# Kernel tuning notes

Measured on AMD Instinct MI355X. Metric: run time of the kernel, lower is better.

The kernel has to match this reference:

```python
import jax, jax.numpy as jnp
import numpy as np

B, T, C = 4, 2048, 1024
H = 16
HD = C // H  # 64


def setup_inputs() -> dict:
    key = jax.random.key(0)
    k1, k2, k3, k4, k5 = jax.random.split(key, 5)
    x = jax.random.normal(k1, (B, T, C), dtype=jnp.float32)
    W_qkv = jax.random.normal(k2, (3 * C, C), dtype=jnp.float32) * (1.0 / np.sqrt(C))
    W_proj = jax.random.normal(k3, (C, C), dtype=jnp.float32) * (1.0 / np.sqrt(C))
    # realistic RoPE tables
    pos = jnp.arange(T, dtype=jnp.float32)[:, None]
    inv_freq = 1.0 / (10000.0 ** (jnp.arange(0, HD, 2, dtype=jnp.float32) / HD))
    ang = pos * inv_freq[None, :]  # [T, HD//2]
    cos = jnp.cos(ang)
    sin = jnp.sin(ang)
    mask = jnp.ones((1, 1, T, T), dtype=jnp.int32)
    return {"x": x, "W_qkv": W_qkv, "W_proj": W_proj, "cos": cos, "sin": sin, "mask": mask}


def _apply_rope(xh, cos, sin):
    # xh: [B, H, T, HD]; cos/sin: [T, HD//2]
    b, h, t, hd = xh.shape
    xr = xh.reshape(b, h, t, hd // 2, 2)
    x1, x2 = xr[..., 0], xr[..., 1]
    c = cos[:t][None, None, :, :]
    s = sin[:t][None, None, :, :]
    o1 = x1 * c - x2 * s
    o2 = x1 * s + x2 * c
    return jnp.stack([o1, o2], axis=-1).reshape(b, h, t, hd)


def reference(x, W_qkv, W_proj, cos, sin, mask):
    b, t, c = x.shape
    qkv = jnp.einsum('btc,dc->btd', x, W_qkv)  # Linear: x @ W^T
    qkv = qkv.reshape(b, t, 3, H, HD).transpose(2, 0, 3, 1, 4)  # [3, B, H, T, HD]
    q, k, v = qkv[0], qkv[1], qkv[2]
    q = _apply_rope(q, cos, sin)
    k = _apply_rope(k, cos, sin)
    scale = 1.0 / np.sqrt(HD)
    attn = jnp.einsum('bhqd,bhkd->bhqk', q, k) * scale
    attn = jnp.where(mask == 0, -jnp.inf, attn)
    attn = jax.nn.softmax(attn, axis=-1)
    out = jnp.einsum('bhqk,bhkd->bhqd', attn, v)
    out = out.transpose(0, 2, 1, 3).reshape(b, t, c)
    out = jnp.einsum('btc,dc->btd', out, W_proj)
    return out
```

## Files before the change

kernel.cpp:

```cpp
#include <hip/hip_runtime.h>
#include <hip/hip_bf16.h>
#include <cstdint>
#include <cstddef>

typedef __attribute__((ext_vector_type(8))) short s16x8;
typedef __attribute__((ext_vector_type(4))) float f32x4;
typedef __attribute__((ext_vector_type(16))) float f32x16;
typedef __attribute__((ext_vector_type(4))) unsigned u32x4;
typedef __attribute__((ext_vector_type(4))) unsigned short us16x4;

#define DEVI static __device__ __forceinline__

DEVI short f2bf(float f) {
  unsigned u = __builtin_bit_cast(unsigned, f);
  u += 0x7fffu + ((u >> 16) & 1u);
  return (short)(u >> 16);
}
DEVI unsigned pack2(float a, float b) {
  return (unsigned)(unsigned short)f2bf(a) | ((unsigned)(unsigned short)f2bf(b) << 16);
}
DEVI f32x4 mfma16(s16x8 a, s16x8 b, f32x4 c) {
  return __builtin_amdgcn_mfma_f32_16x16x32_bf16(a, b, c, 0, 0, 0);
}
DEVI f32x16 mfma32(s16x8 a, s16x8 b, f32x16 c) {
  return __builtin_amdgcn_mfma_f32_32x32x16_bf16(a, b, c, 0, 0, 0);
}
DEVI void gload16(const short* src, short* dst) {
  __builtin_amdgcn_global_load_lds(
      (const __attribute__((address_space(1))) unsigned*)src,
      (__attribute__((address_space(3))) unsigned*)dst, 16, 0, 0);
}
DEVI float expfast(float x) {
  float r; asm("v_exp_f32 %0, %1" : "=v"(r) : "v"(x)); return r;
}
DEVI unsigned cvtpk(float lo, float hi) {
  unsigned r; asm("v_cvt_pk_bf16_f32 %0, %1, %2" : "=v"(r) : "v"(lo), "v"(hi)); return r;
}
DEVI float max3f(float a, float b, float c) {
  float r; asm("v_max3_f32 %0, %1, %2, %3" : "=v"(r) : "v"(a), "v"(b), "v"(c)); return r;
}

__global__ __launch_bounds__(256) void cvt_kernel(
    const float* __restrict__ x, const float* __restrict__ wq,
    const float* __restrict__ wp, short* __restrict__ xb,
    short* __restrict__ wqb, short* __restrict__ wpb)
{
  const long long stride = (long long)gridDim.x * blockDim.x;
  for (long long i = (long long)blockIdx.x * blockDim.x + threadIdx.x;
       i < 1572864; i += stride) {
    const float* src; short* dst; long long off;
    if (i < 1048576)      { src = x;  dst = xb;  off = i; }
    else if (i < 1441792) { src = wq; dst = wqb; off = i - 1048576; }
    else                  { src = wp; dst = wpb; off = i - 1441792; }
    const float4 a = *reinterpret_cast<const float4*>(src + off * 8);
    const float4 b = *reinterpret_cast<const float4*>(src + off * 8 + 4);
    u32x4 o = {pack2(a.x, a.y), pack2(a.z, a.w), pack2(b.x, b.y), pack2(b.z, b.w)};
    *reinterpret_cast<u32x4*>(dst + off * 8) = o;
  }
}

__global__ __launch_bounds__(256, 4) void qkv_rope_b16_kernel(
    const short* __restrict__ xb, const short* __restrict__ wqb,
    const float* __restrict__ cosT, const float* __restrict__ sinT,
    short* __restrict__ qw, short* __restrict__ kw, short* __restrict__ vw)
{
  __shared__ short lds[18432];
  short* const Asb = lds;
  short* const Bsb = lds + 8192;

  const int tid = threadIdx.x;
  const int lane = tid & 63, w = tid >> 6;
  const int wr = w >> 1, wc = w & 1;
  const int l15 = lane & 15, l4 = lane >> 4;

  const int bid = blockIdx.x;
  const int m0 = (bid & 63) * 128;
  const int n0 = (bid >> 6) * 128;

  const int gr = lane >> 2;
  const int scol = ((lane & 3) ^ ((lane >> 3) & 3)) * 8;
  const int rsw = (l15 >> 1) & 3;

  const short* pax = xb + (size_t)(m0 + w * 32 + gr) * 1024 + scol;
  const short* pbx = wqb + (size_t)(n0 + w * 32 + gr) * 1024 + scol;

  auto stage = [&](int buf, int k0) {
    short* la = Asb + buf * 4096 + (w * 32) * 32;
    short* lb = Bsb + buf * 4096 + (w * 32) * 32;
    gload16(pax + k0, la);
    gload16(pax + 16384 + k0, la + 512);
    gload16(pbx + k0, lb);
    gload16(pbx + 16384 + k0, lb + 512);
  };

  f32x4 acc[4][4];
#pragma unroll
  for (int i = 0; i < 4; i++)
#pragma unroll
    for (int j2 = 0; j2 < 4; j2++) acc[i][j2] = (f32x4){0.f, 0.f, 0.f, 0.f};

  stage(0, 0);
  __syncthreads();

#pragma unroll
  for (int t = 0; t < 32; t++) {
    const int cur = t & 1;
    if (t + 1 < 32) stage(cur ^ 1, (t + 1) * 32);
    s16x8 af[4], bf[4];
#pragma unroll
    for (int i = 0; i < 4; i++)
      af[i] = *reinterpret_cast<const s16x8*>(Asb + cur * 4096 + (wr * 64 + i * 16 + l15) * 32 + ((l4 ^ rsw) * 8));
#pragma unroll
    for (int j2 = 0; j2 < 4; j2++)
      bf[j2] = *reinterpret_cast<const s16x8*>(Bsb + cur * 4096 + (wc * 64 + j2 * 16 + l15) * 32 + ((l4 ^ rsw) * 8));
#pragma unroll
    for (int i = 0; i < 4; i++)
#pragma unroll
      for (int j2 = 0; j2 < 4; j2++)
        acc[i][j2] = mfma16(af[i], bf[j2], acc[i][j2]);
    __syncthreads();
  }

  const int three = n0 >> 10;
  short* dst = three == 0 ? qw : (three == 1 ? kw : vw);
  const bool isqk = three < 2;
#pragma unroll
  for (int j2 = 0; j2 < 4; j2++) {
    const int hd = j2 * 16 + l15;
    const int ii = hd >> 1, odd = hd & 1;
#pragma unroll
    for (int i = 0; i < 4; i++) {
#pragma unroll
      for (int r = 0; r < 4; r++) {
        const int tl = wr * 64 + i * 16 + l4 * 4 + r;
        float v = acc[i][j2][r];
        float other = __shfl_xor(v, 1, 64);
        if (isqk) {
          const int trow = (m0 + tl) & 2047;
          float c = cosT[trow * 32 + ii];
          float s = sinT[trow * 32 + ii];
          v = odd ? (other * s + v * c) : (v * c - other * s);
        }
        if (three == 0) v *= 0.18033688f;
        lds[wc * 9216 + tl * 72 + hd] = f2bf(v);
      }
    }
  }
  __syncthreads();
  const int h0 = (n0 >> 6) & 15;
#pragma unroll
  for (int p = 0; p < 8; p++) {
    const int o = (p * 256 + tid) * 8;
    const int hh = o >> 13;
    const int rem = o & 8191;
    const int tl = rem >> 6;
    const int d0 = rem & 63;
    s16x8 vv = *reinterpret_cast<const s16x8*>(lds + hh * 9216 + tl * 72 + d0);
    const int tg = m0 + tl;
    const int b = tg >> 11, trow = tg & 2047;
    const int h = (h0 + hh) & 15;
    *reinterpret_cast<s16x8*>(dst + ((size_t)((b * 16 + h) * 2048 + trow) << 6) + d0) = vv;
  }
}

__global__ __launch_bounds__(256, 4) void proj_b16_kernel(
    const short* __restrict__ ao, const short* __restrict__ wpb,
    float* __restrict__ out)
{
  __shared__ short As[2][128 * 32];
  __shared__ short Bs[2][128 * 32];
  const int tid = threadIdx.x;
  const int lane = tid & 63, w = tid >> 6;
  const int wr = w >> 1, wc = w & 1;
  const int l15 = lane & 15, l4 = lane >> 4;

  const int bid = blockIdx.x;
  const int m0 = (bid & 63) * 128;
  const int n0 = (bid >> 6) * 128;

  const int gr = lane >> 2;
  const int scol = ((lane & 3) ^ ((lane >> 3) & 3)) * 8;
  const int rsw = (l15 >> 1) & 3;

  const short* pax = ao + (size_t)(m0 + w * 32 + gr) * 1024 + scol;
  const short* pbx = wpb + (size_t)(n0 + w * 32 + gr) * 1024 + scol;
  short* const la0 = &As[0][(w * 32) * 32];
  short* const lb0 = &Bs[0][(w * 32) * 32];
  short* const la1 = &As[1][(w * 32) * 32];
  short* const lb1 = &Bs[1][(w * 32) * 32];

  auto stage = [&](int buf, int k0) {
    gload16(pax + k0, buf ? la1 : la0);
    gload16(pax + 16384 + k0, (buf ? la1 : la0) + 512);
    gload16(pbx + k0, buf ? lb1 : lb0);
    gload16(pbx + 16384 + k0, (buf ? lb1 : lb0) + 512);
  };

  f32x4 acc[4][4];
#pragma unroll
  for (int i = 0; i < 4; i++)
#pragma unroll
    for (int j = 0; j < 4; j++) acc[i][j] = (f32x4){0.f, 0.f, 0.f, 0.f};

  stage(0, 0);
  __syncthreads();

#pragma unroll
  for (int t = 0; t < 32; t++) {
    const int cur = t & 1;
    if (t + 1 < 32) stage(cur ^ 1, (t + 1) * 32);
    s16x8 af[4], bf[4];
#pragma unroll
    for (int i = 0; i < 4; i++)
      af[i] = *reinterpret_cast<const s16x8*>(&As[cur][(wr * 64 + i * 16 + l15) * 32 + ((l4 ^ rsw) * 8)]);
#pragma unroll
    for (int j = 0; j < 4; j++)
      bf[j] = *reinterpret_cast<const s16x8*>(&Bs[cur][(wc * 64 + j * 16 + l15) * 32 + ((l4 ^ rsw) * 8)]);
#pragma unroll
    for (int i = 0; i < 4; i++)
#pragma unroll
      for (int j = 0; j < 4; j++)
        acc[i][j] = mfma16(af[i], bf[j], acc[i][j]);
    __syncthreads();
  }

#pragma unroll
  for (int i = 0; i < 4; i++)
#pragma unroll
    for (int j = 0; j < 4; j++)
#pragma unroll
      for (int r = 0; r < 4; r++) {
        int gm = m0 + wr * 64 + i * 16 + l4 * 4 + r;
        int gn = n0 + wc * 64 + j * 16 + l15;
        out[(size_t)gm * 1024 + gn] = acc[i][j][r];
      }
}

__global__ __launch_bounds__(256, 2) void qkv_rope_kernel(
    const float* __restrict__ x, const float* __restrict__ W,
    const float* __restrict__ cosT, const float* __restrict__ sinT,
    short* __restrict__ qw, short* __restrict__ kw, short* __restrict__ vw)
{
  __shared__ short As[128][40];
  __shared__ short Bs[128][40];
  const int tid = threadIdx.x;
  const int lane = tid & 63, w = tid >> 6;
  const int wr = w >> 1, wc = w & 1;
  const int l15 = lane & 15, l4 = lane >> 4;
  const int m0 = blockIdx.x * 128;
  const int n0 = blockIdx.y * 128;

  f32x4 acc[4][4];
#pragma unroll
  for (int i = 0; i < 4; i++)
#pragma unroll
    for (int j = 0; j < 4; j++) acc[i][j] = (f32x4){0.f, 0.f, 0.f, 0.f};

  for (int k0 = 0; k0 < 1024; k0 += 32) {
    if (k0) __syncthreads();
#pragma unroll
    for (int i = 0; i < 4; i++) {
      int c = tid + 256 * i;
      int row = c >> 3, co = (c & 7) * 4;
      const float4 va = *reinterpret_cast<const float4*>(x + (size_t)(m0 + row) * 1024 + k0 + co);
      const float4 vb = *reinterpret_cast<const float4*>(W + (size_t)(n0 + row) * 1024 + k0 + co);
      uint2 pa; pa.x = pack2(va.x, va.y); pa.y = pack2(va.z, va.w);
      uint2 pb; pb.x = pack2(vb.x, vb.y); pb.y = pack2(vb.z, vb.w);
      *reinterpret_cast<uint2*>(&As[row][co]) = pa;
      *reinterpret_cast<uint2*>(&Bs[row][co]) = pb;
    }
    __syncthreads();
    s16x8 af[4], bf[4];
#pragma unroll
    for (int i = 0; i < 4; i++)
      af[i] = *reinterpret_cast<const s16x8*>(&As[wr * 64 + i * 16 + l15][l4 * 8]);
#pragma unroll
    for (int j = 0; j < 4; j++)
      bf[j] = *reinterpret_cast<const s16x8*>(&Bs[wc * 64 + j * 16 + l15][l4 * 8]);
#pragma unroll
    for (int i = 0; i < 4; i++)
#pragma unroll
      for (int j = 0; j < 4; j++)
        acc[i][j] = mfma16(af[i], bf[j], acc[i][j]);
  }

#pragma unroll
  for (int j = 0; j < 4; j++) {
    const int gn = n0 + wc * 64 + j * 16 + l15;
    const int three = gn >> 10;
    const int h = (gn >> 6) & 15;
    const int hd = gn & 63;
    short* dst = three == 0 ? qw : (three == 1 ? kw : vw);
    const bool isqk = three < 2;
    const int ii = hd >> 1;
    const int odd = hd & 1;
#pragma unroll
    for (int i = 0; i < 4; i++) {
#pragma unroll
      for (int r = 0; r < 4; r++) {
        const int gm = m0 + wr * 64 + i * 16 + l4 * 4 + r;
        const int b = gm >> 11;
        const int t = gm & 2047;
        float v = acc[i][j][r];
        float other = __shfl_xor(v, 1, 64);
        if (isqk) {
          float c = cosT[t * 32 + ii];
          float s = sinT[t * 32 + ii];
          v = odd ? (other * s + v * c) : (v * c - other * s);
        }
        if (three == 0) v *= 0.18033688f;
        dst[((size_t)((b * 16 + h) * 2048 + t) << 6) + hd] = f2bf(v);
      }
    }
  }
}

__global__ __launch_bounds__(256, 2) void proj_kernel(
    const short* __restrict__ ao, const float* __restrict__ W, float* __restrict__ out)
{
  __shared__ short As[128][40];
  __shared__ short Bs[128][40];
  const int tid = threadIdx.x;
  const int lane = tid & 63, w = tid >> 6;
  const int wr = w >> 1, wc = w & 1;
  const int l15 = lane & 15, l4 = lane >> 4;
  const int m0 = blockIdx.x * 128;
  const int n0 = blockIdx.y * 128;

  f32x4 acc[4][4];
#pragma unroll
  for (int i = 0; i < 4; i++)
#pragma unroll
    for (int j = 0; j < 4; j++) acc[i][j] = (f32x4){0.f, 0.f, 0.f, 0.f};

  for (int k0 = 0; k0 < 1024; k0 += 32) {
    if (k0) __syncthreads();
#pragma unroll
    for (int i = 0; i < 2; i++) {
      int c = tid + 256 * i;
      int row = c >> 2, co = (c & 3) * 8;
      *reinterpret_cast<s16x8*>(&As[row][co]) =
          *reinterpret_cast<const s16x8*>(ao + (size_t)(m0 + row) * 1024 + k0 + co);
    }
#pragma unroll
    for (int i = 0; i < 4; i++) {
      int c = tid + 256 * i;
      int row = c >> 3, co = (c & 7) * 4;
      const float4 vb = *reinterpret_cast<const float4*>(W + (size_t)(n0 + row) * 1024 + k0 + co);
      uint2 pb; pb.x = pack2(vb.x, vb.y); pb.y = pack2(vb.z, vb.w);
      *reinterpret_cast<uint2*>(&Bs[row][co]) = pb;
    }
    __syncthreads();
    s16x8 af[4], bf[4];
#pragma unroll
    for (int i = 0; i < 4; i++)
      af[i] = *reinterpret_cast<const s16x8*>(&As[wr * 64 + i * 16 + l15][l4 * 8]);
#pragma unroll
    for (int j = 0; j < 4; j++)
      bf[j] = *reinterpret_cast<const s16x8*>(&Bs[wc * 64 + j * 16 + l15][l4 * 8]);
#pragma unroll
    for (int i = 0; i < 4; i++)
#pragma unroll
      for (int j = 0; j < 4; j++)
        acc[i][j] = mfma16(af[i], bf[j], acc[i][j]);
  }

#pragma unroll
  for (int i = 0; i < 4; i++)
#pragma unroll
    for (int j = 0; j < 4; j++)
#pragma unroll
      for (int r = 0; r < 4; r++) {
        int gm = m0 + wr * 64 + i * 16 + l4 * 4 + r;
        int gn = n0 + wc * 64 + j * 16 + l15;
        out[(size_t)gm * 1024 + gn] = acc[i][j][r];
      }
}

__global__ __launch_bounds__(512, 4) void attn_kernel(
    const short* __restrict__ qw, const short* __restrict__ kw,
    const short* __restrict__ vw, short* __restrict__ ao)
{
  __shared__ short lds[24576];
  unsigned* lds32 = (unsigned*)lds;

  const int tid = threadIdx.x;
  const int lane = tid & 63, w = tid >> 6;
  const int l31 = lane & 31, hi = lane >> 5;

  const int fid = blockIdx.y * 8 + blockIdx.x;
  const int qx = (fid >> 3) & 7;
  const int bh = (fid & 7) | ((fid >> 6) << 3);
  const int q0 = qx * 256;
  const size_t base = (size_t)bh << 17;

  const int qrow = q0 + w * 32 + l31;
  s16x8 qf[4];
#pragma unroll
  for (int ds = 0; ds < 4; ds++)
    qf[ds] = *reinterpret_cast<const s16x8*>(qw + base + (size_t)qrow * 64 + ds * 16 + hi * 8);

  const int krow = w * 8 + (lane >> 3);
  const int kslot = lane & 7;
  const int vp = tid & 31;
  const int vd4 = (tid >> 5) * 4;

  auto stageK = [&](int buf, int kv0) {
    short* dst = &lds[buf * 4096 + w * 512];
    const short* src = kw + base + (size_t)(kv0 + krow) * 64 + ((kslot ^ (krow & 7)) * 8);
    gload16(src, dst);
  };
  auto loadV = [&](int kv0, us16x4& lo, us16x4& hi4) {
    const short* s0 = vw + base + (size_t)(kv0 + 2 * vp) * 64 + vd4;
    lo  = *reinterpret_cast<const us16x4*>(s0);
    hi4 = *reinterpret_cast<const us16x4*>(s0 + 64);
  };
  auto writeV = [&](int buf, us16x4 lo, us16x4 hi4) {
#pragma unroll
    for (int i = 0; i < 4; i++) {
      int d = vd4 + i;
      unsigned val = (unsigned)lo[i] | ((unsigned)hi4[i] << 16);
      lds32[4096 + buf * 2048 + d * 32 + (vp ^ ((d & 7) << 2))] = val;
    }
  };

  unsigned* Pw = lds32 + 8192 + w * 512 + l31 * 16;
  const int qsw = (l31 >> 1) & 3;

  f32x16 o0, o1;
#pragma unroll
  for (int r = 0; r < 16; r++) { o0[r] = 0.f; o1[r] = 0.f; }
  float m_run = -1e30f, l_run = 0.f;

  {
    us16x4 lo, hh;
    loadV(0, lo, hh);
    stageK(0, 0);
    writeV(0, lo, hh);
  }
  __syncthreads();

  const int NT = 32;
  for (int kt = 0; kt < NT; kt++) {
    const int cur = kt & 1;
    us16x4 vlo, vhi;
    const bool more = (kt + 1) < NT;
    if (more) {
      loadV((kt + 1) * 64, vlo, vhi);
      stageK(cur ^ 1, (kt + 1) * 64);
    }

    const short* Kbuf = &lds[cur * 4096];
    f32x16 S0, S1;
#pragma unroll
    for (int r = 0; r < 16; r++) { S0[r] = 0.f; S1[r] = 0.f; }
    __builtin_amdgcn_s_setprio(1);
#pragma unroll
    for (int ds = 0; ds < 4; ds++) {
      const int slot = ((ds * 2 + hi) ^ (l31 & 7)) * 8;
      s16x8 a0 = *reinterpret_cast<const s16x8*>(Kbuf + l31 * 64 + slot);
      s16x8 a1 = *reinterpret_cast<const s16x8*>(Kbuf + (32 + l31) * 64 + slot);
      S0 = mfma32(a0, qf[ds], S0);
      S1 = mfma32(a1, qf[ds], S1);
    }
    __builtin_amdgcn_s_setprio(0);

    float a0m = max3f(S0[0], S0[1], S0[2]);
    float a1m = max3f(S0[3], S0[4], S0[5]);
    float a2m = max3f(S0[6], S0[7], S0[8]);
    float a3m = max3f(S0[9], S0[10], S0[11]);
    float a4m = max3f(S0[12], S0[13], S0[14]);
    float a5m = max3f(S0[15], S1[0], S1[1]);
    float a6m = max3f(S1[2], S1[3], S1[4]);
    float a7m = max3f(S1[5], S1[6], S1[7]);
    float a8m = max3f(S1[8], S1[9], S1[10]);
    float a9m = max3f(S1[11], S1[12], S1[13]);
    float aam = fmaxf(S1[14], S1[15]);
    float b0m = max3f(a0m, a1m, a2m);
    float b1m = max3f(a3m, a4m, a5m);
    float b2m = max3f(a6m, a7m, a8m);
    float b3m = fmaxf(a9m, aam);
    float mx = fmaxf(max3f(b0m, b1m, b2m), b3m);
    mx = fmaxf(mx, __shfl_xor(mx, 32, 64));

    if (!__all(mx - m_run <= 8.0f)) {
      const float mnew = fmaxf(m_run, mx);
      const float corr = expfast(m_run - mnew);
      m_run = mnew;
      l_run *= corr;
#pragma unroll
      for (int r = 0; r < 16; r++) { o0[r] *= corr; o1[r] *= corr; }
    }
    float s0a = 0.f, s1a = 0.f, s2a = 0.f, s3a = 0.f;
#pragma unroll
    for (int r = 0; r < 16; r += 4) {
      S0[r+0] = expfast(S0[r+0] - m_run); s0a += S0[r+0];
      S0[r+1] = expfast(S0[r+1] - m_run); s1a += S0[r+1];
      S0[r+2] = expfast(S0[r+2] - m_run); s2a += S0[r+2];
      S0[r+3] = expfast(S0[r+3] - m_run); s3a += S0[r+3];
    }
#pragma unroll
    for (int r = 0; r < 16; r += 4) {
      S1[r+0] = expfast(S1[r+0] - m_run); s0a += S1[r+0];
      S1[r+1] = expfast(S1[r+1] - m_run); s1a += S1[r+1];
      S1[r+2] = expfast(S1[r+2] - m_run); s2a += S1[r+2];
      S1[r+3] = expfast(S1[r+3] - m_run); s3a += S1[r+3];
    }
    float sum = (s0a + s1a) + (s2a + s3a);
    sum += __shfl_xor(sum, 32, 64);
    l_run += sum;

    if (more) writeV(cur ^ 1, vlo, vhi);

    const short* Vbuf = &lds[8192 + cur * 4096];
    auto doHalf = [&](const f32x16& Sh, int sbase) {
      __builtin_amdgcn_s_setprio(1);
#pragma unroll
      for (int g2 = 0; g2 < 4; g2++) {
        uint2 val;
        val.x = cvtpk(Sh[4 * g2 + 0], Sh[4 * g2 + 1]);
        val.y = cvtpk(Sh[4 * g2 + 2], Sh[4 * g2 + 3]);
        *reinterpret_cast<uint2*>(Pw + ((g2 ^ qsw) << 2) + 2 * hi) = val;
      }
#pragma unroll
      for (int sp = 0; sp < 2; sp++) {
        const int s = sbase + sp;
        u32x4 praw = *reinterpret_cast<const u32x4*>(Pw + (((2 * sp + hi) ^ qsw) << 2));
        s16x8 bfrag = __builtin_bit_cast(s16x8, praw);
        const int kvslot = ((s * 2 + hi) ^ (l31 & 7)) * 8;
        s16x8 v0 = *reinterpret_cast<const s16x8*>(Vbuf + l31 * 64 + kvslot);
        s16x8 v1 = *reinterpret_cast<const s16x8*>(Vbuf + (32 + l31) * 64 + kvslot);
        o0 = mfma32(v0, bfrag, o0);
        o1 = mfma32(v1, bfrag, o1);
      }
      __builtin_amdgcn_s_setprio(0);
    };
    doHalf(S0, 0);
    doHalf(S1, 2);

    __syncthreads();
  }

  const float rl = 1.0f / l_run;
  {
    const int q = l31;
#pragma unroll
    for (int dt = 0; dt < 2; dt++) {
#pragma unroll
      for (int rg = 0; rg < 4; rg++) {
        const int d = dt * 32 + 8 * rg + 4 * hi;
        float a0 = (dt ? o1[rg*4+0] : o0[rg*4+0]) * rl;
        float a1 = (dt ? o1[rg*4+1] : o0[rg*4+1]) * rl;
        float a2 = (dt ? o1[rg*4+2] : o0[rg*4+2]) * rl;
        float a3 = (dt ? o1[rg*4+3] : o0[rg*4+3]) * rl;
        const int sidx0 = w * 2048 + q * 64 + (d ^ ((q & 7) << 3));
        const int sidx1 = w * 2048 + q * 64 + ((d + 2) ^ ((q & 7) << 3));
        lds32[sidx0 >> 1] = pack2(a0, a1);
        lds32[sidx1 >> 1] = pack2(a2, a3);
      }
    }
  }
  __syncthreads();
  const int b = bh >> 4, h = bh & 15;
#pragma unroll
  for (int i = 0; i < 4; i++) {
    const int idx = i * 4096 + tid * 8;
    const int wi = idx >> 11;
    const int rem = idx & 2047;
    const int q = rem >> 6;
    const int d8 = rem & 63;
    s16x8 vv = *reinterpret_cast<const s16x8*>(&lds[wi * 2048 + q * 64 + (d8 ^ ((q & 7) << 3))]);
    const int row = q0 + wi * 32 + q;
    *reinterpret_cast<s16x8*>(ao + (size_t)(b * 2048 + row) * 1024 + h * 64 + d8) = vv;
  }
}

extern "C" void kernel_launch(void* const* d_in, const int* in_sizes, int n_in,
                              void* d_out, int out_size, void* d_ws, size_t ws_size,
                              hipStream_t stream) {
  const float* x     = (const float*)d_in[0];
  const float* Wqkv  = (const float*)d_in[1];
  const float* Wproj = (const float*)d_in[2];
  const float* cosT  = (const float*)d_in[3];
  const float* sinT  = (const float*)d_in[4];
  float* out = (float*)d_out;

  const size_t NEL = (size_t)4 * 16 * 2048 * 64;
  short* qw = (short*)d_ws;
  short* kw = qw + NEL;
  short* vw = kw + NEL;
  short* ao = vw + NEL;
  short* xb  = ao + NEL;
  short* wqb = xb + 8388608;
  short* wpb = wqb + 3145728;
  const size_t need = (4 * NEL + 8388608 + 3145728 + 1048576) * sizeof(short);

  if (ws_size >= need) {
    cvt_kernel<<<2048, 256, 0, stream>>>(x, Wqkv, Wproj, xb, wqb, wpb);
    qkv_rope_b16_kernel<<<1536, 256, 0, stream>>>(xb, wqb, cosT, sinT, qw, kw, vw);
    attn_kernel<<<dim3(8, 64), 512, 0, stream>>>(qw, kw, vw, ao);
    proj_b16_kernel<<<512, 256, 0, stream>>>(ao, wpb, out);
  } else {
    qkv_rope_kernel<<<dim3(64, 24), 256, 0, stream>>>(x, Wqkv, cosT, sinT, qw, kw, vw);
    attn_kernel<<<dim3(8, 64), 512, 0, stream>>>(qw, kw, vw, ao);
    proj_kernel<<<dim3(64, 8), 256, 0, stream>>>(ao, Wproj, out);
  }
}
```

Before: 192.9 us.

## Halve attention block size to 128 queries with 4 waves per block

The attention kernel now runs 1024 blocks of 256 threads, each covering 128 query rows, instead of 512 blocks of 512 threads covering 256 rows. K and V staging is redistributed so each thread loads twice as much (two 16-byte K loads and 8-wide V loads), and LDS is shrunk accordingly. The aim is more blocks for better load balance and occupancy across CUs. The cost is that each K/V tile is reused by fewer query rows, so more global and LDS traffic is spent per unit of compute.

```diff
diff --git a/kernel.cpp b/kernel.cpp
--- a/kernel.cpp
+++ b/kernel.cpp
@@ -7,7 +7,6 @@
 typedef __attribute__((ext_vector_type(4))) float f32x4;
 typedef __attribute__((ext_vector_type(16))) float f32x16;
 typedef __attribute__((ext_vector_type(4))) unsigned u32x4;
-typedef __attribute__((ext_vector_type(4))) unsigned short us16x4;
 
 #define DEVI static __device__ __forceinline__
 
@@ -377,21 +376,21 @@
       }
 }
 
-__global__ __launch_bounds__(512, 4) void attn_kernel(
+__global__ __launch_bounds__(256, 4) void attn_kernel(
     const short* __restrict__ qw, const short* __restrict__ kw,
     const short* __restrict__ vw, short* __restrict__ ao)
 {
-  __shared__ short lds[24576];
+  __shared__ short lds[20480];
   unsigned* lds32 = (unsigned*)lds;
 
   const int tid = threadIdx.x;
   const int lane = tid & 63, w = tid >> 6;
   const int l31 = lane & 31, hi = lane >> 5;
 
-  const int fid = blockIdx.y * 8 + blockIdx.x;
-  const int qx = (fid >> 3) & 7;
-  const int bh = (fid & 7) | ((fid >> 6) << 3);
-  const int q0 = qx * 256;
+  const int bid = blockIdx.x;
+  const int qx = (bid >> 3) & 15;
+  const int bh = (bid & 7) | ((bid >> 7) << 3);
+  const int q0 = qx * 128;
   const size_t base = (size_t)bh << 17;
 
   const int qrow = q0 + w * 32 + l31;
@@ -400,26 +399,28 @@
   for (int ds = 0; ds < 4; ds++)
     qf[ds] = *reinterpret_cast<const s16x8*>(qw + base + (size_t)qrow * 64 + ds * 16 + hi * 8);
 
-  const int krow = w * 8 + (lane >> 3);
+  const int krow = w * 16 + (lane >> 3);
   const int kslot = lane & 7;
   const int vp = tid & 31;
-  const int vd4 = (tid >> 5) * 4;
+  const int vd8 = (tid >> 5) * 8;
 
   auto stageK = [&](int buf, int kv0) {
-    short* dst = &lds[buf * 4096 + w * 512];
+    short* dst = &lds[buf * 4096 + w * 1024];
     const short* src = kw + base + (size_t)(kv0 + krow) * 64 + ((kslot ^ (krow & 7)) * 8);
     gload16(src, dst);
+    const short* src2 = kw + base + (size_t)(kv0 + krow + 8) * 64 + ((kslot ^ (krow & 7)) * 8);
+    gload16(src2, dst + 512);
   };
-  auto loadV = [&](int kv0, us16x4& lo, us16x4& hi4) {
-    const short* s0 = vw + base + (size_t)(kv0 + 2 * vp) * 64 + vd4;
-    lo  = *reinterpret_cast<const us16x4*>(s0);
-    hi4 = *reinterpret_cast<const us16x4*>(s0 + 64);
+  auto loadV = [&](int kv0, s16x8& va, s16x8& vb) {
+    const short* s0 = vw + base + (size_t)(kv0 + 2 * vp) * 64 + vd8;
+    va = *reinterpret_cast<const s16x8*>(s0);
+    vb = *reinterpret_cast<const s16x8*>(s0 + 64);
   };
-  auto writeV = [&](int buf, us16x4 lo, us16x4 hi4) {
-#pragma unroll
-    for (int i = 0; i < 4; i++) {
-      int d = vd4 + i;
-      unsigned val = (unsigned)lo[i] | ((unsigned)hi4[i] << 16);
+  auto writeV = [&](int buf, s16x8 va, s16x8 vb) {
+#pragma unroll
+    for (int i = 0; i < 8; i++) {
+      int d = vd8 + i;
+      unsigned val = (unsigned)(unsigned short)va[i] | ((unsigned)(unsigned short)vb[i] << 16);
       lds32[4096 + buf * 2048 + d * 32 + (vp ^ ((d & 7) << 2))] = val;
     }
   };
@@ -433,20 +434,20 @@
   float m_run = -1e30f, l_run = 0.f;
 
   {
-    us16x4 lo, hh;
-    loadV(0, lo, hh);
+    s16x8 va, vb;
+    loadV(0, va, vb);
     stageK(0, 0);
-    writeV(0, lo, hh);
+    writeV(0, va, vb);
   }
   __syncthreads();
 
   const int NT = 32;
   for (int kt = 0; kt < NT; kt++) {
     const int cur = kt & 1;
-    us16x4 vlo, vhi;
+    s16x8 vva, vvb;
     const bool more = (kt + 1) < NT;
     if (more) {
-      loadV((kt + 1) * 64, vlo, vhi);
+      loadV((kt + 1) * 64, vva, vvb);
       stageK(cur ^ 1, (kt + 1) * 64);
     }
 
@@ -510,7 +511,7 @@
     sum += __shfl_xor(sum, 32, 64);
     l_run += sum;
 
-    if (more) writeV(cur ^ 1, vlo, vhi);
+    if (more) writeV(cur ^ 1, vva, vvb);
 
     const short* Vbuf = &lds[8192 + cur * 4096];
     auto doHalf = [&](const f32x16& Sh, int sbase) {
@@ -563,15 +564,15 @@
   __syncthreads();
   const int b = bh >> 4, h = bh & 15;
 #pragma unroll
-  for (int i = 0; i < 4; i++) {
-    const int idx = i * 4096 + tid * 8;
-    const int wi = idx >> 11;
-    const int rem = idx & 2047;
-    const int q = rem >> 6;
-    const int d8 = rem & 63;
+  for (int p = 0; p < 4; p++) {
+    const int idx = (p * 256 + tid) * 8;
+    const int row = idx >> 6;
+    const int wi = row >> 5;
+    const int q = row & 31;
+    const int d8 = idx & 63;
     s16x8 vv = *reinterpret_cast<const s16x8*>(&lds[wi * 2048 + q * 64 + (d8 ^ ((q & 7) << 3))]);
-    const int row = q0 + wi * 32 + q;
-    *reinterpret_cast<s16x8*>(ao + (size_t)(b * 2048 + row) * 1024 + h * 64 + d8) = vv;
+    const int trow = q0 + row;
+    *reinterpret_cast<s16x8*>(ao + (size_t)(b * 2048 + trow) * 1024 + h * 64 + d8) = vv;
   }
 }
 
@@ -598,11 +599,11 @@
   if (ws_size >= need) {
     cvt_kernel<<<2048, 256, 0, stream>>>(x, Wqkv, Wproj, xb, wqb, wpb);
     qkv_rope_b16_kernel<<<1536, 256, 0, stream>>>(xb, wqb, cosT, sinT, qw, kw, vw);
-    attn_kernel<<<dim3(8, 64), 512, 0, stream>>>(qw, kw, vw, ao);
+    attn_kernel<<<1024, 256, 0, stream>>>(qw, kw, vw, ao);
     proj_b16_kernel<<<512, 256, 0, stream>>>(ao, wpb, out);
   } else {
     qkv_rope_kernel<<<dim3(64, 24), 256, 0, stream>>>(x, Wqkv, cosT, sinT, qw, kw, vw);
-    attn_kernel<<<dim3(8, 64), 512, 0, stream>>>(qw, kw, vw, ao);
+    attn_kernel<<<1024, 256, 0, stream>>>(qw, kw, vw, ao);
     proj_kernel<<<dim3(64, 8), 256, 0, stream>>>(ao, Wproj, out);
   }
 }
```

Result: slower. 213.1 us (+10.4%).

## Split attention KV range in two with a combine kernel for more parallelism

Applied to the files above, without the earlier changes.

Adds a split-KV (flash-decoding style) attention path: each block processes half of the key/value sequence for a 256-query tile and writes unnormalized fp32 partial outputs plus running max/sum, and a separate combine kernel merges the two halves into bf16 attention output. This doubles the attention grid from 512 to 1024 blocks to improve occupancy across CUs. In exchange it costs an extra kernel launch and writes and rereads about 64MB of fp32 partials, and it needs a larger workspace, otherwise the old path runs. The fallback GEMM kernels are only moved within the file.

```diff
diff --git a/kernel.cpp b/kernel.cpp
--- a/kernel.cpp
+++ b/kernel.cpp
@@ -236,146 +236,10 @@
       }
 }
 
-__global__ __launch_bounds__(256, 2) void qkv_rope_kernel(
-    const float* __restrict__ x, const float* __restrict__ W,
-    const float* __restrict__ cosT, const float* __restrict__ sinT,
-    short* __restrict__ qw, short* __restrict__ kw, short* __restrict__ vw)
-{
-  __shared__ short As[128][40];
-  __shared__ short Bs[128][40];
-  const int tid = threadIdx.x;
-  const int lane = tid & 63, w = tid >> 6;
-  const int wr = w >> 1, wc = w & 1;
-  const int l15 = lane & 15, l4 = lane >> 4;
-  const int m0 = blockIdx.x * 128;
-  const int n0 = blockIdx.y * 128;
-
-  f32x4 acc[4][4];
-#pragma unroll
-  for (int i = 0; i < 4; i++)
-#pragma unroll
-    for (int j = 0; j < 4; j++) acc[i][j] = (f32x4){0.f, 0.f, 0.f, 0.f};
-
-  for (int k0 = 0; k0 < 1024; k0 += 32) {
-    if (k0) __syncthreads();
-#pragma unroll
-    for (int i = 0; i < 4; i++) {
-      int c = tid + 256 * i;
-      int row = c >> 3, co = (c & 7) * 4;
-      const float4 va = *reinterpret_cast<const float4*>(x + (size_t)(m0 + row) * 1024 + k0 + co);
-      const float4 vb = *reinterpret_cast<const float4*>(W + (size_t)(n0 + row) * 1024 + k0 + co);
-      uint2 pa; pa.x = pack2(va.x, va.y); pa.y = pack2(va.z, va.w);
-      uint2 pb; pb.x = pack2(vb.x, vb.y); pb.y = pack2(vb.z, vb.w);
-      *reinterpret_cast<uint2*>(&As[row][co]) = pa;
-      *reinterpret_cast<uint2*>(&Bs[row][co]) = pb;
-    }
-    __syncthreads();
-    s16x8 af[4], bf[4];
-#pragma unroll
-    for (int i = 0; i < 4; i++)
-      af[i] = *reinterpret_cast<const s16x8*>(&As[wr * 64 + i * 16 + l15][l4 * 8]);
-#pragma unroll
-    for (int j = 0; j < 4; j++)
-      bf[j] = *reinterpret_cast<const s16x8*>(&Bs[wc * 64 + j * 16 + l15][l4 * 8]);
-#pragma unroll
-    for (int i = 0; i < 4; i++)
-#pragma unroll
-      for (int j = 0; j < 4; j++)
-        acc[i][j] = mfma16(af[i], bf[j], acc[i][j]);
-  }
-
-#pragma unroll
-  for (int j = 0; j < 4; j++) {
-    const int gn = n0 + wc * 64 + j * 16 + l15;
-    const int three = gn >> 10;
-    const int h = (gn >> 6) & 15;
-    const int hd = gn & 63;
-    short* dst = three == 0 ? qw : (three == 1 ? kw : vw);
-    const bool isqk = three < 2;
-    const int ii = hd >> 1;
-    const int odd = hd & 1;
-#pragma unroll
-    for (int i = 0; i < 4; i++) {
-#pragma unroll
-      for (int r = 0; r < 4; r++) {
-        const int gm = m0 + wr * 64 + i * 16 + l4 * 4 + r;
-        const int b = gm >> 11;
-        const int t = gm & 2047;
-        float v = acc[i][j][r];
-        float other = __shfl_xor(v, 1, 64);
-        if (isqk) {
-          float c = cosT[t * 32 + ii];
-          float s = sinT[t * 32 + ii];
-          v = odd ? (other * s + v * c) : (v * c - other * s);
-        }
-        if (three == 0) v *= 0.18033688f;
-        dst[((size_t)((b * 16 + h) * 2048 + t) << 6) + hd] = f2bf(v);
-      }
-    }
-  }
-}
-
-__global__ __launch_bounds__(256, 2) void proj_kernel(
-    const short* __restrict__ ao, const float* __restrict__ W, float* __restrict__ out)
-{
-  __shared__ short As[128][40];
-  __shared__ short Bs[128][40];
-  const int tid = threadIdx.x;
-  const int lane = tid & 63, w = tid >> 6;
-  const int wr = w >> 1, wc = w & 1;
-  const int l15 = lane & 15, l4 = lane >> 4;
-  const int m0 = blockIdx.x * 128;
-  const int n0 = blockIdx.y * 128;
-
-  f32x4 acc[4][4];
-#pragma unroll
-  for (int i = 0; i < 4; i++)
-#pragma unroll
-    for (int j = 0; j < 4; j++) acc[i][j] = (f32x4){0.f, 0.f, 0.f, 0.f};
-
-  for (int k0 = 0; k0 < 1024; k0 += 32) {
-    if (k0) __syncthreads();
-#pragma unroll
-    for (int i = 0; i < 2; i++) {
-      int c = tid + 256 * i;
-      int row = c >> 2, co = (c & 3) * 8;
-      *reinterpret_cast<s16x8*>(&As[row][co]) =
-          *reinterpret_cast<const s16x8*>(ao + (size_t)(m0 + row) * 1024 + k0 + co);
-    }
-#pragma unroll
-    for (int i = 0; i < 4; i++) {
-      int c = tid + 256 * i;
-      int row = c >> 3, co = (c & 7) * 4;
-      const float4 vb = *reinterpret_cast<const float4*>(W + (size_t)(n0 + row) * 1024 + k0 + co);
-      uint2 pb; pb.x = pack2(vb.x, vb.y); pb.y = pack2(vb.z, vb.w);
-      *reinterpret_cast<uint2*>(&Bs[row][co]) = pb;
-    }
-    __syncthreads();
-    s16x8 af[4], bf[4];
-#pragma unroll
-    for (int i = 0; i < 4; i++)
-      af[i] = *reinterpret_cast<const s16x8*>(&As[wr * 64 + i * 16 + l15][l4 * 8]);
-#pragma unroll
-    for (int j = 0; j < 4; j++)
-      bf[j] = *reinterpret_cast<const s16x8*>(&Bs[wc * 64 + j * 16 + l15][l4 * 8]);
-#pragma unroll
-    for (int i = 0; i < 4; i++)
-#pragma unroll
-      for (int j = 0; j < 4; j++)
-        acc[i][j] = mfma16(af[i], bf[j], acc[i][j]);
-  }
-
-#pragma unroll
-  for (int i = 0; i < 4; i++)
-#pragma unroll
-    for (int j = 0; j < 4; j++)
-#pragma unroll
-      for (int r = 0; r < 4; r++) {
-        int gm = m0 + wr * 64 + i * 16 + l4 * 4 + r;
-        int gn = n0 + wc * 64 + j * 16 + l15;
-        out[(size_t)gm * 1024 + gn] = acc[i][j][r];
-      }
-}
+struct AttnCore {
+  f32x16 o0, o1;
+  float m_run, l_run;
+};
 
 __global__ __launch_bounds__(512, 4) void attn_kernel(
     const short* __restrict__ qw, const short* __restrict__ kw,
@@ -575,6 +439,382 @@
   }
 }
 
+__global__ __launch_bounds__(512, 4) void attn_split_kernel(
+    const short* __restrict__ qw, const short* __restrict__ kw,
+    const short* __restrict__ vw, float* __restrict__ po0,
+    float* __restrict__ po1, float* __restrict__ ml0,
+    float* __restrict__ ml1)
+{
+  __shared__ short lds[24576];
+  unsigned* lds32 = (unsigned*)lds;
+  float* ldsf = (float*)lds;
+
+  const int tid = threadIdx.x;
+  const int lane = tid & 63, w = tid >> 6;
+  const int l31 = lane & 31, hi = lane >> 5;
+
+  const int bid = blockIdx.x;
+  const int qx = (bid >> 3) & 7;
+  const int sp2 = (bid >> 6) & 1;
+  const int bh = (bid & 7) | ((bid >> 7) << 3);
+  const int q0 = qx * 256;
+  const int kvbase = sp2 * 1024;
+  const size_t base = (size_t)bh << 17;
+
+  float* po = sp2 ? po1 : po0;
+  float* ml = sp2 ? ml1 : ml0;
+
+  const int qrow = q0 + w * 32 + l31;
+  s16x8 qf[4];
+#pragma unroll
+  for (int ds = 0; ds < 4; ds++)
+    qf[ds] = *reinterpret_cast<const s16x8*>(qw + base + (size_t)qrow * 64 + ds * 16 + hi * 8);
+
+  const int krow = w * 8 + (lane >> 3);
+  const int kslot = lane & 7;
+  const int vp = tid & 31;
+  const int vd4 = (tid >> 5) * 4;
+
+  auto stageK = [&](int buf, int kv0) {
+    short* dst = &lds[buf * 4096 + w * 512];
+    const short* src = kw + base + (size_t)(kv0 + krow) * 64 + ((kslot ^ (krow & 7)) * 8);
+    gload16(src, dst);
+  };
+  auto loadV = [&](int kv0, us16x4& lo, us16x4& hi4) {
+    const short* s0 = vw + base + (size_t)(kv0 + 2 * vp) * 64 + vd4;
+    lo  = *reinterpret_cast<const us16x4*>(s0);
+    hi4 = *reinterpret_cast<const us16x4*>(s0 + 64);
+  };
+  auto writeV = [&](int buf, us16x4 lo, us16x4 hi4) {
+#pragma unroll
+    for (int i = 0; i < 4; i++) {
+      int d = vd4 + i;
+      unsigned val = (unsigned)lo[i] | ((unsigned)hi4[i] << 16);
+      lds32[4096 + buf * 2048 + d * 32 + (vp ^ ((d & 7) << 2))] = val;
+    }
+  };
+
+  unsigned* Pw = lds32 + 8192 + w * 512 + l31 * 16;
+  const int qsw = (l31 >> 1) & 3;
+
+  f32x16 o0, o1;
+#pragma unroll
+  for (int r = 0; r < 16; r++) { o0[r] = 0.f; o1[r] = 0.f; }
+  float m_run = -1e30f, l_run = 0.f;
+
+  {
+    us16x4 lo, hh;
+    loadV(kvbase, lo, hh);
+    stageK(0, kvbase);
+    writeV(0, lo, hh);
+  }
+  __syncthreads();
+
+  const int NT = 16;
+  for (int kt = 0; kt < NT; kt++) {
+    const int cur = kt & 1;
+    us16x4 vlo, vhi;
+    const bool more = (kt + 1) < NT;
+    if (more) {
+      loadV(kvbase + (kt + 1) * 64, vlo, vhi);
+      stageK(cur ^ 1, kvbase + (kt + 1) * 64);
+    }
+
+    const short* Kbuf = &lds[cur * 4096];
+    f32x16 S0, S1;
+#pragma unroll
+    for (int r = 0; r < 16; r++) { S0[r] = 0.f; S1[r] = 0.f; }
+    __builtin_amdgcn_s_setprio(1);
+#pragma unroll
+    for (int ds = 0; ds < 4; ds++) {
+      const int slot = ((ds * 2 + hi) ^ (l31 & 7)) * 8;
+      s16x8 a0 = *reinterpret_cast<const s16x8*>(Kbuf + l31 * 64 + slot);
+      s16x8 a1 = *reinterpret_cast<const s16x8*>(Kbuf + (32 + l31) * 64 + slot);
+      S0 = mfma32(a0, qf[ds], S0);
+      S1 = mfma32(a1, qf[ds], S1);
+    }
+    __builtin_amdgcn_s_setprio(0);
+
+    float a0m = max3f(S0[0], S0[1], S0[2]);
+    float a1m = max3f(S0[3], S0[4], S0[5]);
+    float a2m = max3f(S0[6], S0[7], S0[8]);
+    float a3m = max3f(S0[9], S0[10], S0[11]);
+    float a4m = max3f(S0[12], S0[13], S0[14]);
+    float a5m = max3f(S0[15], S1[0], S1[1]);
+    float a6m = max3f(S1[2], S1[3], S1[4]);
+    float a7m = max3f(S1[5], S1[6], S1[7]);
+    float a8m = max3f(S1[8], S1[9], S1[10]);
+    float a9m = max3f(S1[11], S1[12], S1[13]);
+    float aam = fmaxf(S1[14], S1[15]);
+    float b0m = max3f(a0m, a1m, a2m);
+    float b1m = max3f(a3m, a4m, a5m);
+    float b2m = max3f(a6m, a7m, a8m);
+    float b3m = fmaxf(a9m, aam);
+    float mx = fmaxf(max3f(b0m, b1m, b2m), b3m);
+    mx = fmaxf(mx, __shfl_xor(mx, 32, 64));
+
+    if (!__all(mx - m_run <= 8.0f)) {
+      const float mnew = fmaxf(m_run, mx);
+      const float corr = expfast(m_run - mnew);
+      m_run = mnew;
+      l_run *= corr;
+#pragma unroll
+      for (int r = 0; r < 16; r++) { o0[r] *= corr; o1[r] *= corr; }
+    }
+    float s0a = 0.f, s1a = 0.f, s2a = 0.f, s3a = 0.f;
+#pragma unroll
+    for (int r = 0; r < 16; r += 4) {
+      S0[r+0] = expfast(S0[r+0] - m_run); s0a += S0[r+0];
+      S0[r+1] = expfast(S0[r+1] - m_run); s1a += S0[r+1];
+      S0[r+2] = expfast(S0[r+2] - m_run); s2a += S0[r+2];
+      S0[r+3] = expfast(S0[r+3] - m_run); s3a += S0[r+3];
+    }
+#pragma unroll
+    for (int r = 0; r < 16; r += 4) {
+      S1[r+0] = expfast(S1[r+0] - m_run); s0a += S1[r+0];
+      S1[r+1] = expfast(S1[r+1] - m_run); s1a += S1[r+1];
+      S1[r+2] = expfast(S1[r+2] - m_run); s2a += S1[r+2];
+      S1[r+3] = expfast(S1[r+3] - m_run); s3a += S1[r+3];
+    }
+    float sum = (s0a + s1a) + (s2a + s3a);
+    sum += __shfl_xor(sum, 32, 64);
+    l_run += sum;
+
+    if (more) writeV(cur ^ 1, vlo, vhi);
+
+    const short* Vbuf = &lds[8192 + cur * 4096];
+    auto doHalf = [&](const f32x16& Sh, int sbase) {
+      __builtin_amdgcn_s_setprio(1);
+#pragma unroll
+      for (int g2 = 0; g2 < 4; g2++) {
+        uint2 val;
+        val.x = cvtpk(Sh[4 * g2 + 0], Sh[4 * g2 + 1]);
+        val.y = cvtpk(Sh[4 * g2 + 2], Sh[4 * g2 + 3]);
+        *reinterpret_cast<uint2*>(Pw + ((g2 ^ qsw) << 2) + 2 * hi) = val;
+      }
+#pragma unroll
+      for (int spp = 0; spp < 2; spp++) {
+        const int s = sbase + spp;
+        u32x4 praw = *reinterpret_cast<const u32x4*>(Pw + (((2 * spp + hi) ^ qsw) << 2));
+        s16x8 bfrag = __builtin_bit_cast(s16x8, praw);
+        const int kvslot = ((s * 2 + hi) ^ (l31 & 7)) * 8;
+        s16x8 v0 = *reinterpret_cast<const s16x8*>(Vbuf + l31 * 64 + kvslot);
+        s16x8 v1 = *reinterpret_cast<const s16x8*>(Vbuf + (32 + l31) * 64 + kvslot);
+        o0 = mfma32(v0, bfrag, o0);
+        o1 = mfma32(v1, bfrag, o1);
+      }
+      __builtin_amdgcn_s_setprio(0);
+    };
+    doHalf(S0, 0);
+    doHalf(S1, 2);
+
+    __syncthreads();
+  }
+
+  if (hi == 0) {
+    float2 v; v.x = m_run; v.y = l_run;
+    *reinterpret_cast<float2*>(ml + ((size_t)bh * 2048 + q0 + w * 32 + l31) * 2) = v;
+  }
+#pragma unroll
+  for (int dt = 0; dt < 2; dt++) {
+    __syncthreads();
+    const f32x16& oo = dt ? o1 : o0;
+#pragma unroll
+    for (int rg = 0; rg < 4; rg++)
+#pragma unroll
+      for (int j = 0; j < 4; j++) {
+        const int d = 8 * rg + 4 * hi + j;
+        ldsf[w * 1024 + l31 * 32 + (d ^ ((l31 & 7) << 2))] = oo[rg * 4 + j];
+      }
+    __syncthreads();
+#pragma unroll
+    for (int p = 0; p < 4; p++) {
+      const int idx = p * 512 + tid;
+      const int lrow = idx >> 3;
+      const int d4 = (idx & 7) * 4;
+      const int lw = lrow >> 5, lq = lrow & 31;
+      float4 v = *reinterpret_cast<const float4*>(
+          &ldsf[lw * 1024 + lq * 32 + (d4 ^ ((lq & 7) << 2))]);
+      *reinterpret_cast<float4*>(
+          po + ((size_t)bh * 2048 + q0 + lrow) * 64 + dt * 32 + d4) = v;
+    }
+  }
+}
+
+__global__ __launch_bounds__(256) void combine_kernel(
+    const float* __restrict__ po0, const float* __restrict__ po1,
+    const float* __restrict__ ml0, const float* __restrict__ ml1,
+    short* __restrict__ ao)
+{
+  const int idx = blockIdx.x * 256 + threadIdx.x;
+  const int row = idx >> 2;
+  const int qtr = idx & 3;
+  const int d0 = qtr * 16;
+  float2 a = *reinterpret_cast<const float2*>(ml0 + (size_t)row * 2);
+  float2 b = *reinterpret_cast<const float2*>(ml1 + (size_t)row * 2);
+  const float m = fmaxf(a.x, b.x);
+  const float ca = expfast(a.x - m), cb = expfast(b.x - m);
+  const float rl = 1.0f / (a.y * ca + b.y * cb);
+  const float fa = ca * rl, fb = cb * rl;
+  const float* p0 = po0 + (size_t)row * 64 + d0;
+  const float* p1 = po1 + (size_t)row * 64 + d0;
+  const int bh = row >> 11, bb = bh >> 4, h = bh & 15, t = row & 2047;
+  short* dst = ao + ((size_t)(bb * 2048 + t)) * 1024 + h * 64 + d0;
+  unsigned ow[8];
+#pragma unroll
+  for (int g = 0; g < 4; g++) {
+    float4 x = *reinterpret_cast<const float4*>(p0 + g * 4);
+    float4 y = *reinterpret_cast<const float4*>(p1 + g * 4);
+    ow[g * 2 + 0] = pack2(x.x * fa + y.x * fb, x.y * fa + y.y * fb);
+    ow[g * 2 + 1] = pack2(x.z * fa + y.z * fb, x.w * fa + y.w * fb);
+  }
+  u32x4 o1v = {ow[0], ow[1], ow[2], ow[3]};
+  u32x4 o2v = {ow[4], ow[5], ow[6], ow[7]};
+  *reinterpret_cast<u32x4*>(dst) = o1v;
+  *reinterpret_cast<u32x4*>(dst + 8) = o2v;
+}
+
+__global__ __launch_bounds__(256, 2) void qkv_rope_kernel(
+    const float* __restrict__ x, const float* __restrict__ W,
+    const float* __restrict__ cosT, const float* __restrict__ sinT,
+    short* __restrict__ qw, short* __restrict__ kw, short* __restrict__ vw)
+{
+  __shared__ short As[128][40];
+  __shared__ short Bs[128][40];
+  const int tid = threadIdx.x;
+  const int lane = tid & 63, w = tid >> 6;
+  const int wr = w >> 1, wc = w & 1;
+  const int l15 = lane & 15, l4 = lane >> 4;
+  const int m0 = blockIdx.x * 128;
+  const int n0 = blockIdx.y * 128;
+
+  f32x4 acc[4][4];
+#pragma unroll
+  for (int i = 0; i < 4; i++)
+#pragma unroll
+    for (int j = 0; j < 4; j++) acc[i][j] = (f32x4){0.f, 0.f, 0.f, 0.f};
+
+  for (int k0 = 0; k0 < 1024; k0 += 32) {
+    if (k0) __syncthreads();
+#pragma unroll
+    for (int i = 0; i < 4; i++) {
+      int c = tid + 256 * i;
+      int row = c >> 3, co = (c & 7) * 4;
+      const float4 va = *reinterpret_cast<const float4*>(x + (size_t)(m0 + row) * 1024 + k0 + co);
+      const float4 vb = *reinterpret_cast<const float4*>(W + (size_t)(n0 + row) * 1024 + k0 + co);
+      uint2 pa; pa.x = pack2(va.x, va.y); pa.y = pack2(va.z, va.w);
+      uint2 pb; pb.x = pack2(vb.x, vb.y); pb.y = pack2(vb.z, vb.w);
+      *reinterpret_cast<uint2*>(&As[row][co]) = pa;
+      *reinterpret_cast<uint2*>(&Bs[row][co]) = pb;
+    }
+    __syncthreads();
+    s16x8 af[4], bf[4];
+#pragma unroll
+    for (int i = 0; i < 4; i++)
+      af[i] = *reinterpret_cast<const s16x8*>(&As[wr * 64 + i * 16 + l15][l4 * 8]);
+#pragma unroll
+    for (int j = 0; j < 4; j++)
+      bf[j] = *reinterpret_cast<const s16x8*>(&Bs[wc * 64 + j * 16 + l15][l4 * 8]);
+#pragma unroll
+    for (int i = 0; i < 4; i++)
+#pragma unroll
+      for (int j = 0; j < 4; j++)
+        acc[i][j] = mfma16(af[i], bf[j], acc[i][j]);
+  }
+
+#pragma unroll
+  for (int j = 0; j < 4; j++) {
+    const int gn = n0 + wc * 64 + j * 16 + l15;
+    const int three = gn >> 10;
+    const int h = (gn >> 6) & 15;
+    const int hd = gn & 63;
+    short* dst = three == 0 ? qw : (three == 1 ? kw : vw);
+    const bool isqk = three < 2;
+    const int ii = hd >> 1;
+    const int odd = hd & 1;
+#pragma unroll
+    for (int i = 0; i < 4; i++) {
+#pragma unroll
+      for (int r = 0; r < 4; r++) {
+        const int gm = m0 + wr * 64 + i * 16 + l4 * 4 + r;
+        const int b = gm >> 11;
+        const int t = gm & 2047;
+        float v = acc[i][j][r];
+        float other = __shfl_xor(v, 1, 64);
+        if (isqk) {
+          float c = cosT[t * 32 + ii];
+          float s = sinT[t * 32 + ii];
+          v = odd ? (other * s + v * c) : (v * c - other * s);
+        }
+        if (three == 0) v *= 0.18033688f;
+        dst[((size_t)((b * 16 + h) * 2048 + t) << 6) + hd] = f2bf(v);
+      }
+    }
+  }
+}
+
+__global__ __launch_bounds__(256, 2) void proj_kernel(
+    const short* __restrict__ ao, const float* __restrict__ W, float* __restrict__ out)
+{
+  __shared__ short As[128][40];
+  __shared__ short Bs[128][40];
+  const int tid = threadIdx.x;
+  const int lane = tid & 63, w = tid >> 6;
+  const int wr = w >> 1, wc = w & 1;
+  const int l15 = lane & 15, l4 = lane >> 4;
+  const int m0 = blockIdx.x * 128;
+  const int n0 = blockIdx.y * 128;
+
+  f32x4 acc[4][4];
+#pragma unroll
+  for (int i = 0; i < 4; i++)
+#pragma unroll
+    for (int j = 0; j < 4; j++) acc[i][j] = (f32x4){0.f, 0.f, 0.f, 0.f};
+
+  for (int k0 = 0; k0 < 1024; k0 += 32) {
+    if (k0) __syncthreads();
+#pragma unroll
+    for (int i = 0; i < 2; i++) {
+      int c = tid + 256 * i;
+      int row = c >> 2, co = (c & 3) * 8;
+      *reinterpret_cast<s16x8*>(&As[row][co]) =
+          *reinterpret_cast<const s16x8*>(ao + (size_t)(m0 + row) * 1024 + k0 + co);
+    }
+#pragma unroll
+    for (int i = 0; i < 4; i++) {
+      int c = tid + 256 * i;
+      int row = c >> 3, co = (c & 7) * 4;
+      const float4 vb = *reinterpret_cast<const float4*>(W + (size_t)(n0 + row) * 1024 + k0 + co);
+      uint2 pb; pb.x = pack2(vb.x, vb.y); pb.y = pack2(vb.z, vb.w);
+      *reinterpret_cast<uint2*>(&Bs[row][co]) = pb;
+    }
+    __syncthreads();
+    s16x8 af[4], bf[4];
+#pragma unroll
+    for (int i = 0; i < 4; i++)
+      af[i] = *reinterpret_cast<const s16x8*>(&As[wr * 64 + i * 16 + l15][l4 * 8]);
+#pragma unroll
+    for (int j = 0; j < 4; j++)
+      bf[j] = *reinterpret_cast<const s16x8*>(&Bs[wc * 64 + j * 16 + l15][l4 * 8]);
+#pragma unroll
+    for (int i = 0; i < 4; i++)
+#pragma unroll
+      for (int j = 0; j < 4; j++)
+        acc[i][j] = mfma16(af[i], bf[j], acc[i][j]);
+  }
+
+#pragma unroll
+  for (int i = 0; i < 4; i++)
+#pragma unroll
+    for (int j = 0; j < 4; j++)
+#pragma unroll
+      for (int r = 0; r < 4; r++) {
+        int gm = m0 + wr * 64 + i * 16 + l4 * 4 + r;
+        int gn = n0 + wc * 64 + j * 16 + l15;
+        out[(size_t)gm * 1024 + gn] = acc[i][j][r];
+      }
+}
+
 extern "C" void kernel_launch(void* const* d_in, const int* in_sizes, int n_in,
                               void* d_out, int out_size, void* d_ws, size_t ws_size,
                               hipStream_t stream) {
@@ -595,7 +835,19 @@
   short* wpb = wqb + 3145728;
   const size_t need = (4 * NEL + 8388608 + 3145728 + 1048576) * sizeof(short);
 
-  if (ws_size >= need) {
+  float* po0 = (float*)(wpb + 1048576);
+  float* po1 = po0 + 8388608;
+  float* ml0 = po1 + 8388608;
+  float* ml1 = ml0 + 262144;
+  const size_t need_split = need + (2 * 8388608 + 2 * 262144) * sizeof(float);
+
+  if (ws_size >= need_split) {
+    cvt_kernel<<<2048, 256, 0, stream>>>(x, Wqkv, Wproj, xb, wqb, wpb);
+    qkv_rope_b16_kernel<<<1536, 256, 0, stream>>>(xb, wqb, cosT, sinT, qw, kw, vw);
+    attn_split_kernel<<<1024, 512, 0, stream>>>(qw, kw, vw, po0, po1, ml0, ml1);
+    combine_kernel<<<2048, 256, 0, stream>>>(po0, po1, ml0, ml1, ao);
+    proj_b16_kernel<<<512, 256, 0, stream>>>(ao, wpb, out);
+  } else if (ws_size >= need) {
     cvt_kernel<<<2048, 256, 0, stream>>>(x, Wqkv, Wproj, xb, wqb, wpb);
     qkv_rope_b16_kernel<<<1536, 256, 0, stream>>>(xb, wqb, cosT, sinT, qw, kw, vw);
     attn_kernel<<<dim3(8, 64), 512, 0, stream>>>(qw, kw, vw, ao);
```

Result: slower. 211.6 us (+9.7%).
